# Optimization experiments

Measured on AMD Instinct MI355X. Metric: run time of the kernel, lower is better.

The kernel has to match this reference:

```python
import jax, jax.numpy as jnp
import numpy as np

HEADS = 6
HEAD_DIM = 32
DIM = 192
WS = 8            # window size (square)
SHIFTED = True
SCALE = HEAD_DIM ** -0.5


def _rel_indices(wh, ww):
    coords = np.stack(np.meshgrid(np.arange(wh), np.arange(ww), indexing='ij'), -1).reshape(-1, 2)
    rel = coords[:, None, :] - coords[None, :, :]
    return rel[:, :, 0] + wh - 1, rel[:, :, 1] + ww - 1


_REL_H, _REL_W = _rel_indices(WS, WS)  # (WS*WS, WS*WS) int indices, static


def setup_inputs() -> dict:
    key = jax.random.key(0)
    k1, k2, k3, k4, k5 = jax.random.split(key, 5)
    b, h, w = 4, 256, 256
    return {
        'x': jax.random.normal(k1, (b, h, w, DIM), jnp.float32),
        'w_qkv': jax.random.normal(k2, (3 * HEADS * HEAD_DIM, DIM), jnp.float32) * 0.02,
        'pos_embedding': jax.random.normal(k3, (2 * WS - 1, 2 * WS - 1), jnp.float32),
        'w_out': jax.random.normal(k4, (DIM, HEADS * HEAD_DIM), jnp.float32) * 0.02,
        'b_out': jax.random.normal(k5, (DIM,), jnp.float32) * 0.02,
    }


def reference(x, w_qkv, pos_embedding, w_out, b_out):
    disp = WS // 2
    if SHIFTED:
        x = jnp.roll(x, (-disp, -disp), axis=(1, 2))
    b, h, w, _ = x.shape
    nh, nw = h // WS, w // WS

    qkv = jnp.einsum('bhwc,oc->bhwo', x, w_qkv)              # (b,h,w,3*inner)
    qkv = qkv.reshape(b, h, w, 3, HEADS, HEAD_DIM)
    qkv = jnp.transpose(qkv, (3, 0, 4, 1, 2, 5))             # (3,b,H,h,w,d)
    # window partition: (3,b,H,nh,WS,nw,WS,d) -> (3,b,H,nh*nw,WS*WS,d)
    qkv = qkv.reshape(3, b, HEADS, nh, WS, nw, WS, HEAD_DIM)
    qkv = jnp.transpose(qkv, (0, 1, 2, 3, 5, 4, 6, 7))
    qkv = qkv.reshape(3, b, HEADS, nh * nw, WS * WS, HEAD_DIM)
    q, k, v = qkv[0], qkv[1], qkv[2]

    dots = jnp.einsum('bhwid,bhwjd->bhwij', q, k) * SCALE
    dots = dots + pos_embedding[_REL_H, _REL_W]              # gathered rel-pos bias
    attn = jax.nn.softmax(dots, axis=-1)
    out = jnp.einsum('bhwij,bhwjd->bhwid', attn, v)          # (b,H,nw_total,WS*WS,d)

    # un-window: -> (b, h, w, heads*d)
    out = out.reshape(b, HEADS, nh, nw, WS, WS, HEAD_DIM)
    out = jnp.transpose(out, (0, 2, 4, 3, 5, 1, 6))
    out = out.reshape(b, h, w, HEADS * HEAD_DIM)

    out = jnp.einsum('bhwc,oc->bhwo', out, w_out) + b_out
    if SHIFTED:
        out = jnp.roll(out, (disp, disp), axis=(1, 2))
    return out
```

## Files before the change

### kernel.cpp

```cpp
#include <hip/hip_runtime.h>
#include <hip/hip_fp16.h>

typedef __attribute__((ext_vector_type(4))) float     f32x4;
typedef __attribute__((ext_vector_type(8))) _Float16  f16x8;
typedef __attribute__((ext_vector_type(4))) _Float16  f16x4;

#define MFMA(a, b, c) __builtin_amdgcn_mfma_f32_16x16x32_f16(a, b, c, 0, 0, 0)

static constexpr float SCALE = 0.17677669529663687f;
static constexpr float LOG2E = 1.4426950408889634f;

static constexpr unsigned OFF_X    = 0;
static constexpr unsigned OFF_QKV  = 24576;
static constexpr unsigned OFF_P    = 24576 + 73728;
static constexpr unsigned OFF_BIAS = 98304 + 16384;
static constexpr unsigned LDS_BYTES = 131072;

__device__ __forceinline__ unsigned swz(unsigned byte, int row) {
    return byte ^ ((unsigned)(row & 7) << 4);
}

__global__ __launch_bounds__(256)
void wa_prep(const float* __restrict__ wq, const float* __restrict__ wo,
             const float* __restrict__ pos,
             _Float16* __restrict__ wq16, _Float16* __restrict__ wo16,
             float* __restrict__ biasw) {
    const int i = blockIdx.x * 256 + threadIdx.x;
    if (i < 110592) {
        const int e    = i & 7;
        const int lrow = (i >> 3) & 15;
        const int lgrp = (i >> 7) & 3;
        const int ksnt = i >> 9;
        const int ks   = ksnt % 6;
        const int nt   = ksnt / 6;
        const int n = nt * 16 + lrow;
        const int k = ks * 32 + lgrp * 8 + e;
        wq16[i] = (_Float16)wq[n * 192 + k];
    }
    if (i < 36864) {
        const int e    = i & 7;
        const int lrow = (i >> 3) & 15;
        const int lgrp = (i >> 7) & 3;
        const int ksnt = i >> 9;
        const int ks   = ksnt % 6;
        const int nt   = ksnt / 6;
        const int n = nt * 16 + lrow;
        const int k = ks * 32 + lgrp * 8 + e;
        wo16[i] = (_Float16)wo[n * 192 + k];
    }
    if (i < 4096) {
        const int qi = i >> 6, kj = i & 63;
        const int yi = qi >> 3, xi = qi & 7;
        const int yj = kj >> 3, xj = kj & 7;
        biasw[i] = pos[(yi - yj + 7) * 15 + (xi - xj + 7)];
    }
}

__global__ __launch_bounds__(512, 1)
void wa_fused(const float* __restrict__ x,
              const _Float16* __restrict__ wq16,
              const _Float16* __restrict__ wo16,
              const float* __restrict__ b_out,
              const float* __restrict__ biasg,
              float* __restrict__ out) {
    extern __shared__ char smem[];
    const int tid  = threadIdx.x;
    const int lane = tid & 63;
    const int wid  = tid >> 6;
    const int lrow = lane & 15;
    const int lgrp = lane >> 4;

    const int blk = blockIdx.x;
    const int b   = blk >> 10;
    const int wy  = (blk >> 5) & 31;
    const int wx  = blk & 31;

    for (int i = tid; i < 64 * 48; i += 512) {
        const int tok = i / 48;
        const int f4  = i - tok * 48;
        const int ty = tok >> 3, tx = tok & 7;
        const int hh = ((wy << 3) + ty + 4) & 255;
        const int ww = ((wx << 3) + tx + 4) & 255;
        const float4 v = *reinterpret_cast<const float4*>(
            x + ((((size_t)b << 8) + hh) * 256 + ww) * 192 + f4 * 4);
        f16x4 h;
        h[0] = (_Float16)v.x; h[1] = (_Float16)v.y;
        h[2] = (_Float16)v.z; h[3] = (_Float16)v.w;
        *reinterpret_cast<f16x4*>(smem + swz(OFF_X + tok * 384 + f4 * 8, tok)) = h;
    }
    {
        float* bl = reinterpret_cast<float*>(smem + OFF_BIAS);
        for (int i = tid; i < 4096; i += 512) bl[i] = biasg[i];
    }
    __syncthreads();

    {
        const int wm = wid >> 2;
        const int wn = wid & 3;
        f16x8 afr[2][6];
        #pragma unroll
        for (int mt = 0; mt < 2; ++mt) {
            const int row = ((wm * 2 + mt) << 4) + lrow;
            #pragma unroll
            for (int ks = 0; ks < 6; ++ks)
                afr[mt][ks] = *reinterpret_cast<const f16x8*>(
                    smem + swz(OFF_X + row * 384 + ks * 64 + lgrp * 16, row));
        }
        for (int nt0 = 0; nt0 < 9; ++nt0) {
            const int nt = wn * 9 + nt0;
            const _Float16* wbase = wq16 + (size_t)nt * 3072 + lane * 8;
            f32x4 acc0 = {0.f, 0.f, 0.f, 0.f}, acc1 = {0.f, 0.f, 0.f, 0.f};
            #pragma unroll
            for (int ks = 0; ks < 6; ++ks) {
                const f16x8 bfr = *reinterpret_cast<const f16x8*>(wbase + ks * 512);
                acc0 = MFMA(afr[0][ks], bfr, acc0);
                acc1 = MFMA(afr[1][ks], bfr, acc1);
            }
            const int buf   = nt / 12;
            const int head  = (nt % 12) >> 1;
            const int d     = ((nt & 1) << 4) + lrow;
            const unsigned hb = OFF_QKV + head * 12288;
            if (buf < 2) {
                const unsigned base = hb + buf * 4096;
                #pragma unroll
                for (int mt = 0; mt < 2; ++mt) {
                    const f32x4 a = mt ? acc1 : acc0;
                    #pragma unroll
                    for (int r = 0; r < 4; ++r) {
                        const int tok = ((wm * 2 + mt) << 4) + (lgrp << 2) + r;
                        *reinterpret_cast<_Float16*>(
                            smem + swz(base + tok * 64 + d * 2, tok)) = (_Float16)a[r];
                    }
                }
            } else {
                const unsigned base = hb + 8192;
                #pragma unroll
                for (int mt = 0; mt < 2; ++mt) {
                    const f32x4 a = mt ? acc1 : acc0;
                    const int tok0 = ((wm * 2 + mt) << 4) + (lgrp << 2);
                    f16x4 h;
                    #pragma unroll
                    for (int r = 0; r < 4; ++r) h[r] = (_Float16)a[r];
                    *reinterpret_cast<f16x4*>(
                        smem + swz(base + d * 128 + tok0 * 2, d)) = h;
                }
            }
        }
    }
    __syncthreads();

    {
        const float* bl = reinterpret_cast<const float*>(smem + OFF_BIAS);
        const unsigned pbase = OFF_P + wid * 2048;
        for (int u = 0; u < 3; ++u) {
            const int unit  = wid + (u << 3);
            const int head  = unit >> 2;
            const int mtile = unit & 3;
            const unsigned hb = OFF_QKV + head * 12288;

            const int qrow = (mtile << 4) + lrow;
            const f16x8 qa = *reinterpret_cast<const f16x8*>(
                smem + swz(hb + qrow * 64 + lgrp * 16, qrow));
            f32x4 acc[4];
            #pragma unroll
            for (int nt = 0; nt < 4; ++nt) {
                const int krow = (nt << 4) + lrow;
                const f16x8 kb = *reinterpret_cast<const f16x8*>(
                    smem + swz(hb + 4096 + krow * 64 + lgrp * 16, krow));
                const f32x4 z = {0.f, 0.f, 0.f, 0.f};
                acc[nt] = MFMA(qa, kb, z);
            }

            float vals[4][4], mx[4], sm[4];
            #pragma unroll
            for (int r = 0; r < 4; ++r) mx[r] = -1e30f;
            #pragma unroll
            for (int nt = 0; nt < 4; ++nt)
                #pragma unroll
                for (int r = 0; r < 4; ++r) {
                    const float v = acc[nt][r] * SCALE +
                        bl[((mtile << 4) + (lgrp << 2) + r) * 64 + (nt << 4) + lrow];
                    vals[nt][r] = v;
                    mx[r] = fmaxf(mx[r], v);
                }
            #pragma unroll
            for (int m = 1; m < 16; m <<= 1)
                #pragma unroll
                for (int r = 0; r < 4; ++r)
                    mx[r] = fmaxf(mx[r], __shfl_xor(mx[r], m, 64));
            #pragma unroll
            for (int r = 0; r < 4; ++r) sm[r] = 0.f;
            #pragma unroll
            for (int nt = 0; nt < 4; ++nt)
                #pragma unroll
                for (int r = 0; r < 4; ++r) {
                    const float e = exp2f((vals[nt][r] - mx[r]) * LOG2E);
                    vals[nt][r] = e;
                    sm[r] += e;
                }
            #pragma unroll
            for (int m = 1; m < 16; m <<= 1)
                #pragma unroll
                for (int r = 0; r < 4; ++r)
                    sm[r] += __shfl_xor(sm[r], m, 64);

            #pragma unroll
            for (int nt = 0; nt < 4; ++nt)
                #pragma unroll
                for (int r = 0; r < 4; ++r) {
                    const int row = (lgrp << 2) + r;
                    *reinterpret_cast<_Float16*>(
                        smem + swz(pbase + row * 128 + ((nt << 4) + lrow) * 2, row)) =
                        (_Float16)vals[nt][r];
                }
            float rinv[4];
            #pragma unroll
            for (int r = 0; r < 4; ++r) rinv[r] = 1.f / sm[r];

            f32x4 o0 = {0.f, 0.f, 0.f, 0.f}, o1 = {0.f, 0.f, 0.f, 0.f};
            #pragma unroll
            for (int ks = 0; ks < 2; ++ks) {
                const f16x8 pa = *reinterpret_cast<const f16x8*>(
                    smem + swz(pbase + lrow * 128 + ks * 64 + lgrp * 16, lrow));
                const f16x8 vb0 = *reinterpret_cast<const f16x8*>(
                    smem + swz(hb + 8192 + lrow * 128 + ks * 64 + lgrp * 16, lrow));
                const f16x8 vb1 = *reinterpret_cast<const f16x8*>(
                    smem + swz(hb + 8192 + (16 + lrow) * 128 + ks * 64 + lgrp * 16, 16 + lrow));
                o0 = MFMA(pa, vb0, o0);
                o1 = MFMA(pa, vb1, o1);
            }
            #pragma unroll
            for (int r = 0; r < 4; ++r) {
                const int tok = (mtile << 4) + (lgrp << 2) + r;
                const int ch0 = head * 32 + lrow;
                *reinterpret_cast<_Float16*>(
                    smem + swz(OFF_X + tok * 384 + ch0 * 2, tok)) =
                    (_Float16)(o0[r] * rinv[r]);
                *reinterpret_cast<_Float16*>(
                    smem + swz(OFF_X + tok * 384 + (ch0 + 16) * 2, tok)) =
                    (_Float16)(o1[r] * rinv[r]);
            }
        }
    }
    __syncthreads();

    {
        const int wm = wid >> 2;
        const int wn = wid & 3;
        f16x8 afr[2][6];
        #pragma unroll
        for (int mt = 0; mt < 2; ++mt) {
            const int row = ((wm * 2 + mt) << 4) + lrow;
            #pragma unroll
            for (int ks = 0; ks < 6; ++ks)
                afr[mt][ks] = *reinterpret_cast<const f16x8*>(
                    smem + swz(OFF_X + row * 384 + ks * 64 + lgrp * 16, row));
        }
        #pragma unroll
        for (int nt0 = 0; nt0 < 3; ++nt0) {
            const int nt = wn * 3 + nt0;
            const int o  = (nt << 4) + lrow;
            const _Float16* wbase = wo16 + (size_t)nt * 3072 + lane * 8;
            f32x4 acc0 = {0.f, 0.f, 0.f, 0.f}, acc1 = {0.f, 0.f, 0.f, 0.f};
            #pragma unroll
            for (int ks = 0; ks < 6; ++ks) {
                const f16x8 bfr = *reinterpret_cast<const f16x8*>(wbase + ks * 512);
                acc0 = MFMA(afr[0][ks], bfr, acc0);
                acc1 = MFMA(afr[1][ks], bfr, acc1);
            }
            const float bo = b_out[o];
            #pragma unroll
            for (int mt = 0; mt < 2; ++mt) {
                const f32x4 a = mt ? acc1 : acc0;
                #pragma unroll
                for (int r = 0; r < 4; ++r) {
                    const int tok = ((wm * 2 + mt) << 4) + (lgrp << 2) + r;
                    const int ty = tok >> 3, tx = tok & 7;
                    const int hh = ((wy << 3) + ty + 4) & 255;
                    const int ww = ((wx << 3) + tx + 4) & 255;
                    out[((((size_t)b << 8) + hh) * 256 + ww) * 192 + o] = a[r] + bo;
                }
            }
        }
    }
}

extern "C" void kernel_launch(void* const* d_in, const int* in_sizes, int n_in,
                              void* d_out, int out_size, void* d_ws, size_t ws_size,
                              hipStream_t stream) {
    const float* x   = (const float*)d_in[0];
    const float* wq  = (const float*)d_in[1];
    const float* pos = (const float*)d_in[2];
    const float* wo  = (const float*)d_in[3];
    const float* bo  = (const float*)d_in[4];
    float* out = (float*)d_out;

    _Float16* wq16 = (_Float16*)d_ws;
    _Float16* wo16 = (_Float16*)((char*)d_ws + 221184);
    float*    bias = (float*)((char*)d_ws + 221184 + 73728);

    (void)hipFuncSetAttribute((const void*)wa_fused,
                              hipFuncAttributeMaxDynamicSharedMemorySize,
                              (int)LDS_BYTES);

    wa_prep<<<dim3(432), dim3(256), 0, stream>>>(wq, wo, pos, wq16, wo16, bias);
    wa_fused<<<dim3(4096), dim3(512), LDS_BYTES, stream>>>(x, wq16, wo16, bo, bias, out);
}
```

Baseline: 544.5 us.

## Double threads per window block to 16 waves, one M-tile per wave

Raises the fused window-attention block from 8 to 16 wavefronts, so each wave handles one 16-row M tile in the QKV and output projections instead of two. Attention units are spread over 16 waves, with some idle, and the per-wave P scratch area and LDS size grow to fit the extra waves. The aim is more latency hiding per CU, paid for with a larger LDS footprint, more synchronisation participants, and each wave reloading the same weight fragments.

```diff
diff --git a/kernel.cpp b/kernel.cpp
--- a/kernel.cpp
+++ b/kernel.cpp
@@ -13,8 +13,8 @@
 static constexpr unsigned OFF_X    = 0;
 static constexpr unsigned OFF_QKV  = 24576;
 static constexpr unsigned OFF_P    = 24576 + 73728;
-static constexpr unsigned OFF_BIAS = 98304 + 16384;
-static constexpr unsigned LDS_BYTES = 131072;
+static constexpr unsigned OFF_BIAS = 98304 + 32768;
+static constexpr unsigned LDS_BYTES = 131072 + 16384;
 
 __device__ __forceinline__ unsigned swz(unsigned byte, int row) {
     return byte ^ ((unsigned)(row & 7) << 4);
@@ -56,7 +56,7 @@
     }
 }
 
-__global__ __launch_bounds__(512, 1)
+__global__ __launch_bounds__(1024, 1)
 void wa_fused(const float* __restrict__ x,
               const _Float16* __restrict__ wq16,
               const _Float16* __restrict__ wo16,
@@ -75,7 +75,7 @@
     const int wy  = (blk >> 5) & 31;
     const int wx  = blk & 31;
 
-    for (int i = tid; i < 64 * 48; i += 512) {
+    for (int i = tid; i < 64 * 48; i += 1024) {
         const int tok = i / 48;
         const int f4  = i - tok * 48;
         const int ty = tok >> 3, tx = tok & 7;
@@ -90,31 +90,29 @@
     }
     {
         float* bl = reinterpret_cast<float*>(smem + OFF_BIAS);
-        for (int i = tid; i < 4096; i += 512) bl[i] = biasg[i];
+        for (int i = tid; i < 4096; i += 1024) bl[i] = biasg[i];
     }
     __syncthreads();
 
     {
         const int wm = wid >> 2;
         const int wn = wid & 3;
-        f16x8 afr[2][6];
-        #pragma unroll
-        for (int mt = 0; mt < 2; ++mt) {
-            const int row = ((wm * 2 + mt) << 4) + lrow;
+        f16x8 afr[6];
+        {
+            const int row = (wm << 4) + lrow;
             #pragma unroll
             for (int ks = 0; ks < 6; ++ks)
-                afr[mt][ks] = *reinterpret_cast<const f16x8*>(
+                afr[ks] = *reinterpret_cast<const f16x8*>(
                     smem + swz(OFF_X + row * 384 + ks * 64 + lgrp * 16, row));
         }
         for (int nt0 = 0; nt0 < 9; ++nt0) {
             const int nt = wn * 9 + nt0;
             const _Float16* wbase = wq16 + (size_t)nt * 3072 + lane * 8;
-            f32x4 acc0 = {0.f, 0.f, 0.f, 0.f}, acc1 = {0.f, 0.f, 0.f, 0.f};
+            f32x4 acc = {0.f, 0.f, 0.f, 0.f};
             #pragma unroll
             for (int ks = 0; ks < 6; ++ks) {
                 const f16x8 bfr = *reinterpret_cast<const f16x8*>(wbase + ks * 512);
-                acc0 = MFMA(afr[0][ks], bfr, acc0);
-                acc1 = MFMA(afr[1][ks], bfr, acc1);
+                acc = MFMA(afr[ks], bfr, acc);
             }
             const int buf   = nt / 12;
             const int head  = (nt % 12) >> 1;
@@ -123,27 +121,19 @@
             if (buf < 2) {
                 const unsigned base = hb + buf * 4096;
                 #pragma unroll
-                for (int mt = 0; mt < 2; ++mt) {
-                    const f32x4 a = mt ? acc1 : acc0;
-                    #pragma unroll
-                    for (int r = 0; r < 4; ++r) {
-                        const int tok = ((wm * 2 + mt) << 4) + (lgrp << 2) + r;
-                        *reinterpret_cast<_Float16*>(
-                            smem + swz(base + tok * 64 + d * 2, tok)) = (_Float16)a[r];
-                    }
+                for (int r = 0; r < 4; ++r) {
+                    const int tok = (wm << 4) + (lgrp << 2) + r;
+                    *reinterpret_cast<_Float16*>(
+                        smem + swz(base + tok * 64 + d * 2, tok)) = (_Float16)acc[r];
                 }
             } else {
                 const unsigned base = hb + 8192;
-                #pragma unroll
-                for (int mt = 0; mt < 2; ++mt) {
-                    const f32x4 a = mt ? acc1 : acc0;
-                    const int tok0 = ((wm * 2 + mt) << 4) + (lgrp << 2);
-                    f16x4 h;
-                    #pragma unroll
-                    for (int r = 0; r < 4; ++r) h[r] = (_Float16)a[r];
-                    *reinterpret_cast<f16x4*>(
-                        smem + swz(base + d * 128 + tok0 * 2, d)) = h;
-                }
+                const int tok0 = (wm << 4) + (lgrp << 2);
+                f16x4 h;
+                #pragma unroll
+                for (int r = 0; r < 4; ++r) h[r] = (_Float16)acc[r];
+                *reinterpret_cast<f16x4*>(
+                    smem + swz(base + d * 128 + tok0 * 2, d)) = h;
             }
         }
     }
@@ -152,8 +142,9 @@
     {
         const float* bl = reinterpret_cast<const float*>(smem + OFF_BIAS);
         const unsigned pbase = OFF_P + wid * 2048;
-        for (int u = 0; u < 3; ++u) {
-            const int unit  = wid + (u << 3);
+        for (int u = 0; u < 2; ++u) {
+            const int unit = wid + (u << 4);
+            if (unit >= 24) break;
             const int head  = unit >> 2;
             const int mtile = unit & 3;
             const unsigned hb = OFF_QKV + head * 12288;
@@ -247,13 +238,12 @@
     {
         const int wm = wid >> 2;
         const int wn = wid & 3;
-        f16x8 afr[2][6];
-        #pragma unroll
-        for (int mt = 0; mt < 2; ++mt) {
-            const int row = ((wm * 2 + mt) << 4) + lrow;
+        f16x8 afr[6];
+        {
+            const int row = (wm << 4) + lrow;
             #pragma unroll
             for (int ks = 0; ks < 6; ++ks)
-                afr[mt][ks] = *reinterpret_cast<const f16x8*>(
+                afr[ks] = *reinterpret_cast<const f16x8*>(
                     smem + swz(OFF_X + row * 384 + ks * 64 + lgrp * 16, row));
         }
         #pragma unroll
@@ -261,25 +251,20 @@
             const int nt = wn * 3 + nt0;
             const int o  = (nt << 4) + lrow;
             const _Float16* wbase = wo16 + (size_t)nt * 3072 + lane * 8;
-            f32x4 acc0 = {0.f, 0.f, 0.f, 0.f}, acc1 = {0.f, 0.f, 0.f, 0.f};
+            f32x4 acc = {0.f, 0.f, 0.f, 0.f};
             #pragma unroll
             for (int ks = 0; ks < 6; ++ks) {
                 const f16x8 bfr = *reinterpret_cast<const f16x8*>(wbase + ks * 512);
-                acc0 = MFMA(afr[0][ks], bfr, acc0);
-                acc1 = MFMA(afr[1][ks], bfr, acc1);
+                acc = MFMA(afr[ks], bfr, acc);
             }
             const float bo = b_out[o];
             #pragma unroll
-            for (int mt = 0; mt < 2; ++mt) {
-                const f32x4 a = mt ? acc1 : acc0;
-                #pragma unroll
-                for (int r = 0; r < 4; ++r) {
-                    const int tok = ((wm * 2 + mt) << 4) + (lgrp << 2) + r;
-                    const int ty = tok >> 3, tx = tok & 7;
-                    const int hh = ((wy << 3) + ty + 4) & 255;
-                    const int ww = ((wx << 3) + tx + 4) & 255;
-                    out[((((size_t)b << 8) + hh) * 256 + ww) * 192 + o] = a[r] + bo;
-                }
+            for (int r = 0; r < 4; ++r) {
+                const int tok = (wm << 4) + (lgrp << 2) + r;
+                const int ty = tok >> 3, tx = tok & 7;
+                const int hh = ((wy << 3) + ty + 4) & 255;
+                const int ww = ((wx << 3) + tx + 4) & 255;
+                out[((((size_t)b << 8) + hh) * 256 + ww) * 192 + o] = acc[r] + bo;
             }
         }
     }
@@ -304,5 +289,5 @@
                               (int)LDS_BYTES);
 
     wa_prep<<<dim3(432), dim3(256), 0, stream>>>(wq, wo, pos, wq16, wo16, bias);
-    wa_fused<<<dim3(4096), dim3(512), LDS_BYTES, stream>>>(x, wq16, wo16, bo, bias, out);
-}
+    wa_fused<<<dim3(4096), dim3(1024), LDS_BYTES, stream>>>(x, wq16, wo16, bo, bias, out);
+}
```

Measured after the change: 546.2 us. No clear change (+0.3%).
